# Kernel tuning notes

Hardware: AMD Instinct MI355X
Metric: run time of the kernel (lower is better)

## Reference

```python
import jax, jax.numpy as jnp
import numpy as np

B, S, HID, NH, INTER = 1, 2048, 1024, 16, 4096
D = INTER // NH  # per-head intermediate dim = 256


def setup_inputs() -> dict:
    key = jax.random.key(0)
    ks = jax.random.split(key, 10)
    w = lambda k, shp: jax.random.normal(k, shp, jnp.float32) * 0.02
    return {
        "x": jax.random.normal(ks[0], (B, S, HID), jnp.float32),
        "adjacency": jax.random.uniform(ks[1], (B, NH, S, S), jnp.float32),
        "Wg": w(ks[2], (INTER, HID)),   # gate_proj.weight (out,in)
        "Wu": w(ks[3], (INTER, HID)),   # up_proj.weight
        "Wd": w(ks[4], (HID, INTER)),   # down_proj.weight
        "eps": jnp.zeros((NH,), jnp.float32),   # GIN epsilons (init 0)
        "alpha": jnp.ones((NH,), jnp.float32),  # sum-agg scales (init 1)
        "Wq": w(ks[5], (NH, D, D)),     # per-head attn_query_projs weights (out,in)
        "Wk": w(ks[6], (NH, D, D)),     # per-head attn_key_projs weights
        "W1": w(ks[7], (D, 4 * D)),     # aggregator_mlp[0].weight
        "W2": w(ks[8], (D, D)),         # aggregator_mlp[2].weight
    }


def reference(x, adjacency, Wg, Wu, Wd, eps, alpha, Wq, Wk, W1, W2):
    b, s, _ = x.shape
    nh, d, _ = Wq.shape
    # first half of SwiGLU MLP
    h = jax.nn.silu(x @ Wg.T) * (x @ Wu.T)            # (b, s, inter)
    h = h.reshape(b, s, nh, d).transpose(0, 2, 1, 3)  # (b, h, s, d)
    # GIN original term
    orig = (1.0 + eps)[None, :, None, None] * h
    # sum aggregation over adjacency
    sum_agg = alpha[None, :, None, None] * jnp.einsum('bhij,bhjd->bhid', adjacency, h)
    # max over identical expanded copies of h along the neighbor axis == h itself
    max_agg = h
    # adjacency-log-masked attention aggregation
    Q = jnp.einsum('bhsd,hed->bhse', h, Wq)
    K = jnp.einsum('bhsd,hed->bhse', h, Wk)
    scores = jnp.einsum('bhse,bhte->bhst', Q, K) / jnp.sqrt(jnp.float32(d))
    scores = scores + jnp.log(adjacency + 1e-9)
    attn = jax.nn.softmax(scores, axis=-1)
    attn_agg = jnp.einsum('bhst,bhtd->bhsd', attn, h)
    # 4-way concat + aggregator MLP (per head, shared weights)
    comb = jnp.concatenate([orig, sum_agg, max_agg, attn_agg], axis=-1)  # (b,h,s,4d)
    gin = jnp.einsum('bhsd,od->bhso', jax.nn.silu(jnp.einsum('bhsi,oi->bhso', comb, W1)), W2)
    # recombine heads and finish MLP
    gin = gin.transpose(0, 2, 1, 3).reshape(b, s, nh * d)
    return gin @ Wd.T
```

## Files before the change

kernel.cpp:

```cpp
#include <hip/hip_runtime.h>

typedef unsigned short u16;
typedef __attribute__((ext_vector_type(4))) float f32x4;
typedef __attribute__((ext_vector_type(8))) short s16x8;
typedef __attribute__((ext_vector_type(4))) short s16x4;

#define DEVI static __device__ __forceinline__

constexpr int S = 2048, HID = 1024, NH = 16, D = 256, INTER = 4096;

constexpr size_t N_XB   = (size_t)S*HID;
constexpr size_t N_W    = (size_t)INTER*HID;
constexpr size_t N_WQK  = (size_t)NH*D*D;
constexpr size_t N_W1C  = (size_t)NH*D*768;
constexpr size_t N_W2   = (size_t)D*D;
constexpr size_t N_COMB = (size_t)NH*S*768;
constexpr size_t N_HB   = (size_t)NH*S*D;

constexpr size_t O_XB   = 0;
constexpr size_t O_WG   = O_XB + N_XB;
constexpr size_t O_WU   = O_WG + N_W;
constexpr size_t O_WD   = O_WU + N_W;
constexpr size_t O_WQ   = O_WD + N_W;
constexpr size_t O_WK   = O_WQ + N_WQK;
constexpr size_t O_W1C  = O_WK + N_WQK;
constexpr size_t O_W2   = O_W1C + N_W1C;
constexpr size_t O_COMB = O_W2 + N_W2;
constexpr size_t O_HB   = O_COMB + N_COMB;
constexpr size_t O_QB   = O_HB + N_HB;
constexpr size_t O_KC   = O_QB + N_HB;

DEVI u16 f2bf(float f) {
  union { float f; unsigned u; } v; v.f = f;
  unsigned r = v.u + 0x7FFFu + ((v.u >> 16) & 1u);
  return (u16)(r >> 16);
}

DEVI float bf2f(u16 b) {
  union { unsigned u; float f; } v; v.u = ((unsigned)b) << 16;
  return v.f;
}

DEVI void gload16(const void* g, const void* l) {
  __builtin_amdgcn_global_load_lds(
      (const __attribute__((address_space(1))) unsigned int*)g,
      (__attribute__((address_space(3))) unsigned int*)l, 16, 0, 0);
}

DEVI void stage_rm(const u16* src, int stride, u16* lds, int tid) {
  const int wid = tid >> 6;
#pragma unroll
  for (int i = 0; i < 2; ++i) {
    int c = i * 256 + tid;
    gload16(src + (size_t)(c & 127) * stride + (c >> 7) * 8,
            lds + (size_t)(i * 256 + wid * 64) * 8);
  }
}

DEVI void stage_rm64(const u16* src, int stride, u16* lds, int tid) {
  const int wid = tid >> 6;
  gload16(src + (size_t)(tid & 63) * stride + (tid >> 6) * 8,
          lds + (size_t)(wid * 64) * 8);
}

DEVI s16x8 ldfrag(const u16* lds, int kp, int row) {
  return *(const s16x8*)(lds + ((size_t)kp * 128 + row) * 8);
}

DEVI s16x8 ldfrag64(const u16* lds, int kp, int row) {
  return *(const s16x8*)(lds + ((size_t)kp * 64 + row) * 8);
}

__global__ void k_convert(const float* __restrict__ x,  const float* __restrict__ Wg,
                          const float* __restrict__ Wu, const float* __restrict__ Wd,
                          const float* __restrict__ Wq, const float* __restrict__ Wk,
                          const float* __restrict__ W1, const float* __restrict__ W2,
                          const float* __restrict__ eps, const float* __restrict__ alpha,
                          u16* __restrict__ ws) {
  const size_t total = N_XB + N_W + N_W + N_W + N_WQK + N_WQK + N_W2 + N_W1C;
  for (size_t i = (size_t)blockIdx.x * blockDim.x + threadIdx.x; i < total;
       i += (size_t)gridDim.x * blockDim.x) {
    size_t j = i;
    if (j < N_XB)  { ws[O_XB + j] = f2bf(x[j]);  continue; } j -= N_XB;
    if (j < N_W)   { ws[O_WG + j] = f2bf(Wg[j]); continue; } j -= N_W;
    if (j < N_W)   { ws[O_WU + j] = f2bf(Wu[j]); continue; } j -= N_W;
    if (j < N_W)   { ws[O_WD + j] = f2bf(Wd[j]); continue; } j -= N_W;
    if (j < N_WQK) { ws[O_WQ + j] = f2bf(Wq[j]); continue; } j -= N_WQK;
    if (j < N_WQK) { ws[O_WK + j] = f2bf(Wk[j]); continue; } j -= N_WQK;
    if (j < N_W2)  { ws[O_W2 + j] = f2bf(W2[(j % D) * D + (j / D)]); continue; } j -= N_W2;
    size_t h = j / ((size_t)D * 768);
    size_t r = j % ((size_t)D * 768);
    size_t o = r / 768, c = r % 768;
    float v;
    if (c < 256)      v = (1.f + eps[h]) * W1[o * 1024 + c] + W1[o * 1024 + 512 + c];
    else if (c < 512) v = alpha[h] * W1[o * 1024 + c];
    else              v = W1[o * 1024 + 256 + c];
    ws[O_W1C + j] = f2bf(v);
  }
}

template <int MODE>
__global__ __launch_bounds__(256, 2) void k_dual(const u16* __restrict__ Ab,
                                                 const u16* __restrict__ B0b,
                                                 const u16* __restrict__ B1b,
                                                 u16* __restrict__ o0, u16* __restrict__ o1) {
  __shared__ u16 lA[4096], lB0[4096], lB1[4096];
  const int tid = threadIdx.x, lane = tid & 63, wid = tid >> 6;
  const int wm = wid >> 1, wn = wid & 1;
  const int m0 = blockIdx.x * 128, nt = blockIdx.y, head = blockIdx.z;

  const int K  = (MODE == 0) ? HID : D;
  const int sA = (MODE == 0) ? HID : 768;
  const int sB = (MODE == 0) ? HID : D;
  const u16* A  = (MODE == 0) ? (Ab + (size_t)m0 * HID)
                              : (Ab + ((size_t)head * S + m0) * 768);
  const u16* B0 = (MODE == 0) ? (B0b + (size_t)nt * 128 * HID)
                              : (B0b + (size_t)head * D * D + (size_t)nt * 128 * D);
  const u16* B1 = (MODE == 0) ? (B1b + (size_t)nt * 128 * HID)
                              : (B1b + (size_t)head * D * D + (size_t)nt * 128 * D);

  f32x4 a0[4][4], a1[4][4];
#pragma unroll
  for (int i = 0; i < 4; ++i)
#pragma unroll
    for (int j = 0; j < 4; ++j) { a0[i][j] = f32x4{0.f,0.f,0.f,0.f}; a1[i][j] = f32x4{0.f,0.f,0.f,0.f}; }

  for (int k0 = 0; k0 < K; k0 += 32) {
    __syncthreads();
    stage_rm(A  + k0, sA, lA,  tid);
    stage_rm(B0 + k0, sB, lB0, tid);
    stage_rm(B1 + k0, sB, lB1, tid);
    __syncthreads();
    const int kp = lane >> 4, r = lane & 15;
    s16x8 af[4], b0f[4], b1f[4];
#pragma unroll
    for (int f = 0; f < 4; ++f) {
      af[f]  = ldfrag(lA,  kp, wm * 64 + f * 16 + r);
      b0f[f] = ldfrag(lB0, kp, wn * 64 + f * 16 + r);
      b1f[f] = ldfrag(lB1, kp, wn * 64 + f * 16 + r);
    }
#pragma unroll
    for (int fi = 0; fi < 4; ++fi)
#pragma unroll
      for (int fj = 0; fj < 4; ++fj) {
        a0[fi][fj] = __builtin_amdgcn_mfma_f32_16x16x32_bf16(af[fi], b0f[fj], a0[fi][fj], 0, 0, 0);
        a1[fi][fj] = __builtin_amdgcn_mfma_f32_16x16x32_bf16(af[fi], b1f[fj], a1[fi][fj], 0, 0, 0);
      }
  }

#pragma unroll
  for (int fi = 0; fi < 4; ++fi)
#pragma unroll
    for (int fj = 0; fj < 4; ++fj)
#pragma unroll
      for (int reg = 0; reg < 4; ++reg) {
        int row = m0 + wm * 64 + fi * 16 + ((lane >> 4) * 4 + reg);
        int cl  = wn * 64 + fj * 16 + (lane & 15);
        if (MODE == 0) {
          int col = nt * 128 + cl;
          float g = a0[fi][fj][reg], uu = a1[fi][fj][reg];
          float h = g / (1.f + __expf(-g)) * uu;
          u16 hb = f2bf(h);
          int hh = col >> 8, d = col & 255;
          o0[((size_t)hh * S + row) * 768 + d] = hb;
          o1[(((size_t)hh * (S / 8) + (row >> 3)) * 256 + d) * 8 + (row & 7)] = hb;
        } else {
          int e = nt * 128 + cl;
          o0[((size_t)head * S + row) * D + e] = f2bf(a0[fi][fj][reg]);
          o1[(((size_t)head * 32 + (e >> 3)) * S + row) * 8 + (e & 7)] = f2bf(a1[fi][fj][reg]);
        }
      }
}

__global__ __launch_bounds__(256, 2) void k_attn(const float* __restrict__ adj,
                                                 const u16* __restrict__ Qb,
                                                 const u16* __restrict__ Kc,
                                                 const u16* __restrict__ hB,
                                                 u16* __restrict__ comb) {
  __shared__ u16 lK[2][1024 * 8];
  __shared__ u16 lH[2][1024 * 8];
  __shared__ u16 lAdj[2][64 * 36];
  __shared__ u16 lP[4][16 * 36];
  const int tid = threadIdx.x, lane = tid & 63, wid = tid >> 6;
  const int head = blockIdx.y;
  const int q0 = blockIdx.x * 64 + wid * 16;
  const int l15 = lane & 15, l4 = lane >> 4;

  s16x8 q[8];
  {
    const u16* qr = Qb + ((size_t)head * S + q0 + l15) * D + l4 * 8;
#pragma unroll
    for (int ks = 0; ks < 8; ++ks) q[ks] = *(const s16x8*)(qr + ks * 32);
  }
  f32x4 accO[16], accS[16];
#pragma unroll
  for (int i = 0; i < 16; ++i) { accO[i] = f32x4{0.f,0.f,0.f,0.f}; accS[i] = f32x4{0.f,0.f,0.f,0.f}; }
  float m_r[4] = {-1e30f, -1e30f, -1e30f, -1e30f};
  float l_r[4] = {0.f, 0.f, 0.f, 0.f};

  const float* adjB = adj + ((size_t)head * S + blockIdx.x * 64) * S;
  const int arow = tid >> 3;
  const int acol = (tid & 7) * 4;

#pragma unroll
  for (int i = 0; i < 4; ++i) {
    int c = i * 256 + tid;
    gload16(Kc + ((size_t)(head * 32 + (c >> 5)) * S + (c & 31)) * 8,
            &lK[0][(size_t)(i * 256 + wid * 64) * 8]);
  }
#pragma unroll
  for (int i = 0; i < 4; ++i) {
    int c = i * 256 + tid;
    gload16(hB + ((size_t)(head * (S / 8) + (c >> 8)) * 256 + (c & 255)) * 8,
            &lH[0][(size_t)(i * 256 + wid * 64) * 8]);
  }
  f32x4 av0 = *(const f32x4*)(adjB + (size_t)arow * S + acol);
  f32x4 av1 = *(const f32x4*)(adjB + (size_t)(arow + 32) * S + acol);

  auto TILE = [&](int t0, int cur) {
    const int t1 = (t0 + 32 < S) ? t0 + 32 : t0;
#pragma unroll
    for (int i = 0; i < 4; ++i) {
      int c = i * 256 + tid;
      gload16(Kc + ((size_t)(head * 32 + (c >> 5)) * S + t1 + (c & 31)) * 8,
              &lK[cur ^ 1][(size_t)(i * 256 + wid * 64) * 8]);
    }
#pragma unroll
    for (int i = 0; i < 4; ++i) {
      int c = i * 256 + tid;
      gload16(hB + ((size_t)(head * (S / 8) + (t1 >> 3) + (c >> 8)) * 256 + (c & 255)) * 8,
              &lH[cur ^ 1][(size_t)(i * 256 + wid * 64) * 8]);
    }
    f32x4 nv0 = *(const f32x4*)(adjB + (size_t)arow * S + t1 + acol);
    f32x4 nv1 = *(const f32x4*)(adjB + (size_t)(arow + 32) * S + t1 + acol);
    {
      s16x4 w;
      w[0] = (short)f2bf(av0[0]); w[1] = (short)f2bf(av0[1]);
      w[2] = (short)f2bf(av0[2]); w[3] = (short)f2bf(av0[3]);
      *(s16x4*)(&lAdj[cur][(size_t)arow * 36 + acol]) = w;
      w[0] = (short)f2bf(av1[0]); w[1] = (short)f2bf(av1[1]);
      w[2] = (short)f2bf(av1[2]); w[3] = (short)f2bf(av1[3]);
      *(s16x4*)(&lAdj[cur][(size_t)(arow + 32) * 36 + acol]) = w;
    }
    asm volatile("s_waitcnt vmcnt(10) lgkmcnt(0)" ::: "memory");
    __builtin_amdgcn_s_barrier();
    __builtin_amdgcn_sched_barrier(0);

    const u16* lKc = &lK[cur][0];
    const u16* lHc = &lH[cur][0];
    const u16* lAc = &lAdj[cur][0];

    f32x4 scA[2], scB[2];
    scA[0] = f32x4{0.f,0.f,0.f,0.f}; scA[1] = f32x4{0.f,0.f,0.f,0.f};
    scB[0] = f32x4{0.f,0.f,0.f,0.f}; scB[1] = f32x4{0.f,0.f,0.f,0.f};
#pragma unroll
    for (int ks = 0; ks < 4; ++ks)
#pragma unroll
      for (int fj = 0; fj < 2; ++fj) {
        s16x8 b0 = *(const s16x8*)(lKc + ((size_t)(ks * 4 + l4) * 32 + fj * 16 + l15) * 8);
        s16x8 b1 = *(const s16x8*)(lKc + ((size_t)((ks + 4) * 4 + l4) * 32 + fj * 16 + l15) * 8);
        scA[fj] = __builtin_amdgcn_mfma_f32_16x16x32_bf16(q[ks], b0, scA[fj], 0, 0, 0);
        scB[fj] = __builtin_amdgcn_mfma_f32_16x16x32_bf16(q[ks + 4], b1, scB[fj], 0, 0, 0);
      }

    float av[2][4];
#pragma unroll
    for (int fj = 0; fj < 2; ++fj)
#pragma unroll
      for (int reg = 0; reg < 4; ++reg)
        av[fj][reg] = bf2f(lAc[(size_t)(wid * 16 + l4 * 4 + reg) * 36 + fj * 16 + l15]);

    float sf[2][4];
#pragma unroll
    for (int fj = 0; fj < 2; ++fj)
#pragma unroll
      for (int reg = 0; reg < 4; ++reg)
        sf[fj][reg] = (scA[fj][reg] + scB[fj][reg]) * 0.0625f;

    bool chg = false;
    float lmax[4];
#pragma unroll
    for (int reg = 0; reg < 4; ++reg) {
      lmax[reg] = fmaxf(sf[0][reg], sf[1][reg]);
      chg |= (lmax[reg] > m_r[reg] + 8.f);
    }
    if (__any((int)chg)) {
      float scl[4];
#pragma unroll
      for (int reg = 0; reg < 4; ++reg) {
        float m = lmax[reg];
#pragma unroll
        for (int off = 1; off < 16; off <<= 1) m = fmaxf(m, __shfl_xor(m, off));
        float mn = fmaxf(m_r[reg], m);
        scl[reg] = __expf(m_r[reg] - mn);
        m_r[reg] = mn;
        l_r[reg] *= scl[reg];
      }
#pragma unroll
      for (int nf = 0; nf < 16; ++nf) {
        f32x4 t = accO[nf];
        t[0] *= scl[0]; t[1] *= scl[1]; t[2] *= scl[2]; t[3] *= scl[3];
        accO[nf] = t;
      }
    }
    u16 pb[2][4];
#pragma unroll
    for (int fj = 0; fj < 2; ++fj)
#pragma unroll
      for (int reg = 0; reg < 4; ++reg) {
        float p = (av[fj][reg] + 1e-9f) * exp2f((sf[fj][reg] - m_r[reg]) * 1.44269504f);
        l_r[reg] += p;
        pb[fj][reg] = f2bf(p);
      }

    u16* pl = &lP[wid][0];
#pragma unroll
    for (int fj = 0; fj < 2; ++fj)
#pragma unroll
      for (int reg = 0; reg < 4; ++reg)
        pl[(size_t)(l4 * 4 + reg) * 36 + fj * 16 + l15] = pb[fj][reg];
    asm volatile("s_waitcnt lgkmcnt(0)" ::: "memory");
    __builtin_amdgcn_sched_barrier(0);

    s16x8 pa, aa;
    {
      s16x4 plo = *(const s16x4*)(pl + (size_t)l15 * 36 + l4 * 8);
      s16x4 phi = *(const s16x4*)(pl + (size_t)l15 * 36 + l4 * 8 + 4);
      pa[0] = plo[0]; pa[1] = plo[1]; pa[2] = plo[2]; pa[3] = plo[3];
      pa[4] = phi[0]; pa[5] = phi[1]; pa[6] = phi[2]; pa[7] = phi[3];
      s16x4 alo = *(const s16x4*)(lAc + (size_t)(wid * 16 + l15) * 36 + l4 * 8);
      s16x4 ahi = *(const s16x4*)(lAc + (size_t)(wid * 16 + l15) * 36 + l4 * 8 + 4);
      aa[0] = alo[0]; aa[1] = alo[1]; aa[2] = alo[2]; aa[3] = alo[3];
      aa[4] = ahi[0]; aa[5] = ahi[1]; aa[6] = ahi[2]; aa[7] = ahi[3];
    }
#pragma unroll
    for (int nf = 0; nf < 16; ++nf) {
      s16x8 hb = *(const s16x8*)(lHc + ((size_t)l4 * 256 + nf * 16 + l15) * 8);
      accO[nf] = __builtin_amdgcn_mfma_f32_16x16x32_bf16(pa, hb, accO[nf], 0, 0, 0);
      accS[nf] = __builtin_amdgcn_mfma_f32_16x16x32_bf16(aa, hb, accS[nf], 0, 0, 0);
    }

    av0 = nv0; av1 = nv1;

    __builtin_amdgcn_sched_barrier(0);
    __builtin_amdgcn_s_barrier();
  };

  for (int t0 = 0; t0 < S; t0 += 64) {
    TILE(t0, 0);
    TILE(t0 + 32, 1);
  }

  asm volatile("s_waitcnt vmcnt(0)" ::: "memory");

#pragma unroll
  for (int reg = 0; reg < 4; ++reg) {
#pragma unroll
    for (int off = 1; off < 16; off <<= 1) l_r[reg] += __shfl_xor(l_r[reg], off);
  }
  float inv[4];
#pragma unroll
  for (int reg = 0; reg < 4; ++reg) inv[reg] = 1.f / l_r[reg];
#pragma unroll
  for (int nf = 0; nf < 16; ++nf)
#pragma unroll
    for (int reg = 0; reg < 4; ++reg) {
      size_t rb = ((size_t)head * S + q0 + l4 * 4 + reg) * 768;
      comb[rb + 512 + nf * 16 + l15] = f2bf(accO[nf][reg] * inv[reg]);
      comb[rb + 256 + nf * 16 + l15] = f2bf(accS[nf][reg]);
    }
}

template <int MODE>
__global__ __launch_bounds__(256, 2) void k_gemm(const u16* __restrict__ Ab,
                                                 const u16* __restrict__ Bb,
                                                 u16* __restrict__ oU, float* __restrict__ oF) {
  constexpr int BN = (MODE == 2) ? 64 : 128;
  constexpr int FJ = BN / 32;
  __shared__ u16 lA[4096], lB[BN * 32];
  const int tid = threadIdx.x, lane = tid & 63, wid = tid >> 6;
  const int wm = wid >> 1, wn = wid & 1;
  const int m0 = blockIdx.x * 128, nt = blockIdx.y, head = blockIdx.z;

  constexpr int K  = (MODE == 0) ? 768 : (MODE == 2) ? INTER : D;
  constexpr int sA = (MODE == 3) ? INTER : K;
  constexpr int sB = K;
  const u16* A = (MODE == 0) ? Ab + ((size_t)head * S + m0) * 768
               : (MODE == 2) ? Ab + (size_t)m0 * INTER
                             : Ab + (size_t)m0 * INTER + head * D;
  const u16* B = (MODE == 0) ? Bb + ((size_t)head * D + nt * 128) * 768
                             : Bb + (size_t)nt * BN * sB;

  f32x4 acc[4][FJ];
#pragma unroll
  for (int i = 0; i < 4; ++i)
#pragma unroll
    for (int j = 0; j < FJ; ++j) acc[i][j] = f32x4{0.f,0.f,0.f,0.f};

  for (int k0 = 0; k0 < K; k0 += 32) {
    __syncthreads();
    stage_rm(A + k0, sA, lA, tid);
    if constexpr (BN == 128) stage_rm(B + k0, sB, lB, tid);
    else                     stage_rm64(B + k0, sB, lB, tid);
    __syncthreads();
    const int kp = lane >> 4, r = lane & 15;
    s16x8 af[4], bf[FJ];
#pragma unroll
    for (int f = 0; f < 4; ++f) af[f] = ldfrag(lA, kp, wm * 64 + f * 16 + r);
#pragma unroll
    for (int f = 0; f < FJ; ++f) {
      if constexpr (BN == 128) bf[f] = ldfrag(lB, kp, wn * 64 + f * 16 + r);
      else                     bf[f] = ldfrag64(lB, kp, wn * 32 + f * 16 + r);
    }
#pragma unroll
    for (int fi = 0; fi < 4; ++fi)
#pragma unroll
      for (int fj = 0; fj < FJ; ++fj)
        acc[fi][fj] = __builtin_amdgcn_mfma_f32_16x16x32_bf16(af[fi], bf[fj], acc[fi][fj], 0, 0, 0);
  }

#pragma unroll
  for (int fi = 0; fi < 4; ++fi)
#pragma unroll
    for (int fj = 0; fj < FJ; ++fj)
#pragma unroll
      for (int reg = 0; reg < 4; ++reg) {
        int row = m0 + wm * 64 + fi * 16 + ((lane >> 4) * 4 + reg);
        int cn = nt * BN + wn * (BN / 2) + fj * 16 + (lane & 15);
        float v = acc[fi][fj][reg];
        if (MODE == 0) {
          v = v / (1.f + __expf(-v));
          oU[(size_t)row * INTER + head * D + cn] = f2bf(v);
        } else if (MODE == 3) {
          oU[(size_t)row * INTER + head * D + cn] = f2bf(v);
        } else {
          oF[(size_t)row * HID + cn] = v;
        }
      }
}

extern "C" void kernel_launch(void* const* d_in, const int* in_sizes, int n_in,
                              void* d_out, int out_size, void* d_ws, size_t ws_size,
                              hipStream_t stream) {
  const float* x     = (const float*)d_in[0];
  const float* adj   = (const float*)d_in[1];
  const float* Wg    = (const float*)d_in[2];
  const float* Wu    = (const float*)d_in[3];
  const float* Wd    = (const float*)d_in[4];
  const float* eps   = (const float*)d_in[5];
  const float* alpha = (const float*)d_in[6];
  const float* Wq    = (const float*)d_in[7];
  const float* Wk    = (const float*)d_in[8];
  const float* W1    = (const float*)d_in[9];
  const float* W2    = (const float*)d_in[10];
  u16* ws = (u16*)d_ws;

  k_convert<<<dim3(4096), dim3(256), 0, stream>>>(x, Wg, Wu, Wd, Wq, Wk, W1, W2, eps, alpha, ws);
  k_dual<0><<<dim3(16, 32, 1), dim3(256), 0, stream>>>(ws + O_XB, ws + O_WG, ws + O_WU,
                                                       ws + O_COMB, ws + O_HB);
  k_dual<1><<<dim3(16, 2, 16), dim3(256), 0, stream>>>(ws + O_COMB, ws + O_WQ, ws + O_WK,
                                                       ws + O_QB, ws + O_KC);
  k_attn<<<dim3(32, 16), dim3(256), 0, stream>>>(adj, ws + O_QB, ws + O_KC, ws + O_HB, ws + O_COMB);
  k_gemm<3><<<dim3(8, 2, 16), dim3(256), 0, stream>>>(ws + O_WD, ws + O_W2, ws + O_KC, nullptr);
  k_gemm<0><<<dim3(16, 2, 16), dim3(256), 0, stream>>>(ws + O_COMB, ws + O_W1C, ws + O_QB, nullptr);
  k_gemm<2><<<dim3(16, 16, 1), dim3(256), 0, stream>>>(ws + O_QB, ws + O_KC, nullptr, (float*)d_out);
}
```

Measured before the change: 422.5 us.

## Vectorize fp32-to-bf16 conversion, remap attention blocks per XCD, nontemporal adjacency loads

The conversion kernel now handles x, Wg, Wu, Wd, Wq and Wk four floats at a time with a vector load and a packed bf16 store. The transposed W2 and the combined W1 stay on the scalar path. The attention kernel switches to a 1D grid whose block index is remapped so that blocks of the same head are grouped by block-index modulo 8, which likely targets MI355X's per-XCD L2 reuse of K and h tiles. Adjacency is read with nontemporal loads so this large stream-once tensor is less likely to evict reused data from cache.

```diff
diff --git a/kernel.cpp b/kernel.cpp
--- a/kernel.cpp
+++ b/kernel.cpp
@@ -47,6 +47,10 @@
       (__attribute__((address_space(3))) unsigned int*)l, 16, 0, 0);
 }
 
+DEVI f32x4 ntload(const float* p) {
+  return __builtin_nontemporal_load((const f32x4*)p);
+}
+
 DEVI void stage_rm(const u16* src, int stride, u16* lds, int tid) {
   const int wid = tid >> 6;
 #pragma unroll
@@ -77,17 +81,28 @@
                           const float* __restrict__ W1, const float* __restrict__ W2,
                           const float* __restrict__ eps, const float* __restrict__ alpha,
                           u16* __restrict__ ws) {
-  const size_t total = N_XB + N_W + N_W + N_W + N_WQK + N_WQK + N_W2 + N_W1C;
-  for (size_t i = (size_t)blockIdx.x * blockDim.x + threadIdx.x; i < total;
+  const size_t totv = (N_XB + 3 * N_W + 2 * N_WQK) / 4;
+  for (size_t vi = (size_t)blockIdx.x * blockDim.x + threadIdx.x; vi < totv;
+       vi += (size_t)gridDim.x * blockDim.x) {
+    size_t j = vi * 4;
+    const float* src; size_t dst;
+    if (j < N_XB)                { src = x  + j;                    dst = O_XB + j; }
+    else if ((j -= N_XB) < N_W)  { src = Wg + j;                    dst = O_WG + j; }
+    else if ((j -= N_W) < N_W)   { src = Wu + j;                    dst = O_WU + j; }
+    else if ((j -= N_W) < N_W)   { src = Wd + j;                    dst = O_WD + j; }
+    else if ((j -= N_W) < N_WQK) { src = Wq + j;                    dst = O_WQ + j; }
+    else   { j -= N_WQK;           src = Wk + j;                    dst = O_WK + j; }
+    f32x4 v = *(const f32x4*)src;
+    s16x4 w;
+    w[0] = (short)f2bf(v[0]); w[1] = (short)f2bf(v[1]);
+    w[2] = (short)f2bf(v[2]); w[3] = (short)f2bf(v[3]);
+    *(s16x4*)(ws + dst) = w;
+  }
+  const size_t tot2 = N_W2 + N_W1C;
+  for (size_t i = (size_t)blockIdx.x * blockDim.x + threadIdx.x; i < tot2;
        i += (size_t)gridDim.x * blockDim.x) {
     size_t j = i;
-    if (j < N_XB)  { ws[O_XB + j] = f2bf(x[j]);  continue; } j -= N_XB;
-    if (j < N_W)   { ws[O_WG + j] = f2bf(Wg[j]); continue; } j -= N_W;
-    if (j < N_W)   { ws[O_WU + j] = f2bf(Wu[j]); continue; } j -= N_W;
-    if (j < N_W)   { ws[O_WD + j] = f2bf(Wd[j]); continue; } j -= N_W;
-    if (j < N_WQK) { ws[O_WQ + j] = f2bf(Wq[j]); continue; } j -= N_WQK;
-    if (j < N_WQK) { ws[O_WK + j] = f2bf(Wk[j]); continue; } j -= N_WQK;
-    if (j < N_W2)  { ws[O_W2 + j] = f2bf(W2[(j % D) * D + (j / D)]); continue; } j -= N_W2;
+    if (j < N_W2) { ws[O_W2 + j] = f2bf(W2[(j % D) * D + (j / D)]); continue; } j -= N_W2;
     size_t h = j / ((size_t)D * 768);
     size_t r = j % ((size_t)D * 768);
     size_t o = r / 768, c = r % 768;
@@ -182,8 +197,12 @@
   __shared__ u16 lAdj[2][64 * 36];
   __shared__ u16 lP[4][16 * 36];
   const int tid = threadIdx.x, lane = tid & 63, wid = tid >> 6;
-  const int head = blockIdx.y;
-  const int q0 = blockIdx.x * 64 + wid * 16;
+  const int bid  = blockIdx.x;
+  const int slot = bid & 7;
+  const int idx  = bid >> 3;
+  const int head = slot + 8 * (idx >> 5);
+  const int bx   = idx & 31;
+  const int q0 = bx * 64 + wid * 16;
   const int l15 = lane & 15, l4 = lane >> 4;
 
   s16x8 q[8];
@@ -198,7 +217,7 @@
   float m_r[4] = {-1e30f, -1e30f, -1e30f, -1e30f};
   float l_r[4] = {0.f, 0.f, 0.f, 0.f};
 
-  const float* adjB = adj + ((size_t)head * S + blockIdx.x * 64) * S;
+  const float* adjB = adj + ((size_t)head * S + bx * 64) * S;
   const int arow = tid >> 3;
   const int acol = (tid & 7) * 4;
 
@@ -214,8 +233,8 @@
     gload16(hB + ((size_t)(head * (S / 8) + (c >> 8)) * 256 + (c & 255)) * 8,
             &lH[0][(size_t)(i * 256 + wid * 64) * 8]);
   }
-  f32x4 av0 = *(const f32x4*)(adjB + (size_t)arow * S + acol);
-  f32x4 av1 = *(const f32x4*)(adjB + (size_t)(arow + 32) * S + acol);
+  f32x4 av0 = ntload(adjB + (size_t)arow * S + acol);
+  f32x4 av1 = ntload(adjB + (size_t)(arow + 32) * S + acol);
 
   auto TILE = [&](int t0, int cur) {
     const int t1 = (t0 + 32 < S) ? t0 + 32 : t0;
@@ -231,8 +250,8 @@
       gload16(hB + ((size_t)(head * (S / 8) + (t1 >> 3) + (c >> 8)) * 256 + (c & 255)) * 8,
               &lH[cur ^ 1][(size_t)(i * 256 + wid * 64) * 8]);
     }
-    f32x4 nv0 = *(const f32x4*)(adjB + (size_t)arow * S + t1 + acol);
-    f32x4 nv1 = *(const f32x4*)(adjB + (size_t)(arow + 32) * S + t1 + acol);
+    f32x4 nv0 = ntload(adjB + (size_t)arow * S + t1 + acol);
+    f32x4 nv1 = ntload(adjB + (size_t)(arow + 32) * S + t1 + acol);
     {
       s16x4 w;
       w[0] = (short)f2bf(av0[0]); w[1] = (short)f2bf(av0[1]);
@@ -460,7 +479,7 @@
                                                        ws + O_COMB, ws + O_HB);
   k_dual<1><<<dim3(16, 2, 16), dim3(256), 0, stream>>>(ws + O_COMB, ws + O_WQ, ws + O_WK,
                                                        ws + O_QB, ws + O_KC);
-  k_attn<<<dim3(32, 16), dim3(256), 0, stream>>>(adj, ws + O_QB, ws + O_KC, ws + O_HB, ws + O_COMB);
+  k_attn<<<dim3(512), dim3(256), 0, stream>>>(adj, ws + O_QB, ws + O_KC, ws + O_HB, ws + O_COMB);
   k_gemm<3><<<dim3(8, 2, 16), dim3(256), 0, stream>>>(ws + O_WD, ws + O_W2, ws + O_KC, nullptr);
   k_gemm<0><<<dim3(16, 2, 16), dim3(256), 0, stream>>>(ws + O_COMB, ws + O_W1C, ws + O_QB, nullptr);
   k_gemm<2><<<dim3(16, 16, 1), dim3(256), 0, stream>>>(ws + O_QB, ws + O_KC, nullptr, (float*)d_out);
```

New measurement: 385.0 us. 8.9% less time.
